# Kernel tuning notes

Measured on AMD Instinct MI355X. Metric: run time of the kernel, lower is better.

Reference implementation:

```python
import jax, jax.numpy as jnp
import numpy as np

N_NODES = 100000
N_EDGES = 1600000
IN_F = 512
OUT_F = 256
ORDER = 2


def setup_inputs() -> dict:
    key = jax.random.key(0)
    k1, k2, k3, k4, k5 = jax.random.split(key, 5)
    features = jax.random.normal(k1, (N_NODES, IN_F), dtype=jnp.float32)
    # Xavier-uniform init like torch.nn.init.xavier_uniform_
    limit = float(np.sqrt(6.0 / (IN_F + OUT_F)))
    weight = jax.random.uniform(k2, (IN_F, OUT_F), dtype=jnp.float32, minval=-limit, maxval=limit)
    row = jnp.sort(jax.random.randint(k3, (N_EDGES,), 0, N_NODES, dtype=jnp.int32))
    col = jax.random.randint(k4, (N_EDGES,), 0, N_NODES, dtype=jnp.int32)
    adj_vals = jax.random.uniform(k5, (N_EDGES,), dtype=jnp.float32)
    return {"features": features, "weight": weight, "row": row, "col": col, "adj_vals": adj_vals}


def _spmm(row, col, vals, x, n):
    # out[i] = sum_{e: row[e]==i} vals[e] * x[col[e]]  (COO sparse @ dense)
    msgs = vals[:, None] * x[col]  # [E, F]
    return jax.ops.segment_sum(msgs, row, num_segments=n)


def reference(features, weight, row, col, adj_vals):
    out = jnp.tanh(features @ weight)  # dense mm + tanh (active=True)
    for _ in range(ORDER):  # spmm once, then order-1 more times
        out = _spmm(row, col, adj_vals, out, N_NODES)
    return out
```

## Files before the change

### kernel.cpp

```cpp
#include <hip/hip_runtime.h>
#include <hip/hip_bf16.h>

#define M_NODES 100000
#define N_EDGES 1600000
#define K_IN 512
#define N_OUT 256

typedef short bf16x8 __attribute__((ext_vector_type(8)));
typedef float f32x4 __attribute__((ext_vector_type(4)));

#define GLOBAL_AS __attribute__((address_space(1)))
#define LDS_AS __attribute__((address_space(3)))

__device__ inline unsigned short f2bf_u(float f) {
  union { float f; unsigned u; } x; x.f = f;
  unsigned r = x.u + 0x7FFFu + ((x.u >> 16) & 1u);
  return (unsigned short)(r >> 16);
}
__device__ inline float bfu2f(unsigned short h) {
  union { unsigned u; float f; } x; x.u = ((unsigned)h) << 16;
  return x.f;
}

__global__ void prep_w_kernel(const float* __restrict__ w, short* __restrict__ wt) {
  int idx = blockIdx.x * 256 + threadIdx.x;
  int k = idx >> 8, n = idx & 255;
  wt[n * K_IN + k] = (short)f2bf_u(w[idx]);
}

__global__ void build_rp_kernel(const int* __restrict__ row, int* __restrict__ rp) {
  int r = blockIdx.x * 256 + threadIdx.x;
  if (r > M_NODES) return;
  int lo = 0, hi = N_EDGES;
  while (lo < hi) {
    int mid = (lo + hi) >> 1;
    if (row[mid] < r) lo = mid + 1; else hi = mid;
  }
  rp[r] = lo;
}

__global__ __launch_bounds__(256) void gemm_tanh_kernel(
    const float* __restrict__ A, const short* __restrict__ Wt,
    unsigned short* __restrict__ H) {
  __shared__ __align__(16) short As[64 * 64];
  __shared__ __align__(16) short Bs[256 * 64];
  const int tid = threadIdx.x;
  const int wave = tid >> 6, lane = tid & 63;
  const int quad = lane >> 4, l16 = lane & 15;
  const int row0 = blockIdx.x * 64;

  f32x4 acc[16];
  #pragma unroll
  for (int i = 0; i < 16; ++i) acc[i] = (f32x4){0.f, 0.f, 0.f, 0.f};

  const int ra = tid >> 2;
  const int kb = (tid & 3) << 4;
  const int gr = min(row0 + ra, M_NODES - 1);
  const float* Arow = A + (size_t)gr * K_IN;

  for (int k0 = 0; k0 < K_IN; k0 += 64) {
    #pragma unroll
    for (int it = 0; it < 8; ++it) {
      int g = wave * 512 + it * 64 + lane;
      int n = g >> 3, phys = g & 7;
      int j = phys ^ (n & 7);
      const short* gp = Wt + (size_t)n * K_IN + k0 + j * 8;
      __builtin_amdgcn_global_load_lds(
          (GLOBAL_AS const void*)gp,
          (LDS_AS void*)&Bs[(wave * 512 + it * 64) * 8],
          16, 0, 0);
    }
    float4 a0 = *(const float4*)&Arow[k0 + kb];
    float4 a1 = *(const float4*)&Arow[k0 + kb + 4];
    float4 a2 = *(const float4*)&Arow[k0 + kb + 8];
    float4 a3 = *(const float4*)&Arow[k0 + kb + 12];
    union { unsigned short s[16]; int4 v[2]; } u;
    u.s[0]=f2bf_u(a0.x); u.s[1]=f2bf_u(a0.y); u.s[2]=f2bf_u(a0.z); u.s[3]=f2bf_u(a0.w);
    u.s[4]=f2bf_u(a1.x); u.s[5]=f2bf_u(a1.y); u.s[6]=f2bf_u(a1.z); u.s[7]=f2bf_u(a1.w);
    u.s[8]=f2bf_u(a2.x); u.s[9]=f2bf_u(a2.y); u.s[10]=f2bf_u(a2.z); u.s[11]=f2bf_u(a2.w);
    u.s[12]=f2bf_u(a3.x); u.s[13]=f2bf_u(a3.y); u.s[14]=f2bf_u(a3.z); u.s[15]=f2bf_u(a3.w);
    int lc0 = kb >> 3;
    #pragma unroll
    for (int c = 0; c < 2; ++c) {
      int phys = (lc0 + c) ^ (ra & 7);
      *(int4*)&As[ra * 64 + phys * 8] = u.v[c];
    }
    __syncthreads();
    const int r = wave * 16 + l16;
    #pragma unroll
    for (int kstep = 0; kstep < 2; ++kstep) {
      int lc = kstep * 4 + quad;
      bf16x8 af = *(const bf16x8*)&As[r * 64 + (lc ^ (r & 7)) * 8];
      #pragma unroll
      for (int nt = 0; nt < 16; ++nt) {
        int n = nt * 16 + l16;
        bf16x8 bfr = *(const bf16x8*)&Bs[n * 64 + (lc ^ (n & 7)) * 8];
        acc[nt] = __builtin_amdgcn_mfma_f32_16x16x32_bf16(af, bfr, acc[nt], 0, 0, 0);
      }
    }
    __syncthreads();
  }
  #pragma unroll
  for (int nt = 0; nt < 16; ++nt) {
    #pragma unroll
    for (int rr = 0; rr < 4; ++rr) {
      int row = row0 + wave * 16 + quad * 4 + rr;
      if (row < M_NODES) {
        H[(size_t)row * N_OUT + nt * 16 + l16] = f2bf_u(tanhf(acc[nt][rr]));
      }
    }
  }
}

__global__ __launch_bounds__(256) void spmm_bf_bf(
    const int* __restrict__ rp, const int* __restrict__ colv,
    const float* __restrict__ vals, const unsigned short* __restrict__ x,
    unsigned short* __restrict__ y) {
  int w = (blockIdx.x * 256 + threadIdx.x) >> 6;
  int lane = threadIdx.x & 63;
  int i = __builtin_amdgcn_readfirstlane(w);
  int s = rp[i], e = rp[i + 1];
  float a0 = 0.f, a1 = 0.f, a2 = 0.f, a3 = 0.f;
  const unsigned short* xl = x + lane * 4;
  for (int base = s; base < e; base += 64) {
    int nn = min(e - base, 64);
    int tl = min(base + lane, e - 1);
    int c_l = colv[tl];
    float v_l = vals[tl];
    int tt = 0;
    for (; tt + 8 <= nn; tt += 8) {
      ushort4 xv[8]; float vv[8];
      #pragma unroll
      for (int j = 0; j < 8; ++j) {
        int c = __shfl(c_l, tt + j);
        vv[j] = __shfl(v_l, tt + j);
        xv[j] = *(const ushort4*)(xl + (size_t)c * N_OUT);
      }
      #pragma unroll
      for (int j = 0; j < 8; ++j) {
        a0 += vv[j] * bfu2f(xv[j].x); a1 += vv[j] * bfu2f(xv[j].y);
        a2 += vv[j] * bfu2f(xv[j].z); a3 += vv[j] * bfu2f(xv[j].w);
      }
    }
    for (; tt + 4 <= nn; tt += 4) {
      ushort4 xv[4]; float vv[4];
      #pragma unroll
      for (int j = 0; j < 4; ++j) {
        int c = __shfl(c_l, tt + j);
        vv[j] = __shfl(v_l, tt + j);
        xv[j] = *(const ushort4*)(xl + (size_t)c * N_OUT);
      }
      #pragma unroll
      for (int j = 0; j < 4; ++j) {
        a0 += vv[j] * bfu2f(xv[j].x); a1 += vv[j] * bfu2f(xv[j].y);
        a2 += vv[j] * bfu2f(xv[j].z); a3 += vv[j] * bfu2f(xv[j].w);
      }
    }
    for (; tt < nn; ++tt) {
      int c = __shfl(c_l, tt);
      float v = __shfl(v_l, tt);
      ushort4 xv = *(const ushort4*)(xl + (size_t)c * N_OUT);
      a0 += v * bfu2f(xv.x); a1 += v * bfu2f(xv.y);
      a2 += v * bfu2f(xv.z); a3 += v * bfu2f(xv.w);
    }
  }
  ushort4 o;
  o.x = f2bf_u(a0); o.y = f2bf_u(a1); o.z = f2bf_u(a2); o.w = f2bf_u(a3);
  *(ushort4*)(y + (size_t)i * N_OUT + lane * 4) = o;
}

__global__ __launch_bounds__(256) void spmm_bf_f32(
    const int* __restrict__ rp, const int* __restrict__ colv,
    const float* __restrict__ vals, const unsigned short* __restrict__ x,
    float* __restrict__ y) {
  int w = (blockIdx.x * 256 + threadIdx.x) >> 6;
  int lane = threadIdx.x & 63;
  int i = __builtin_amdgcn_readfirstlane(w);
  int s = rp[i], e = rp[i + 1];
  float a0 = 0.f, a1 = 0.f, a2 = 0.f, a3 = 0.f;
  const unsigned short* xl = x + lane * 4;
  for (int base = s; base < e; base += 64) {
    int nn = min(e - base, 64);
    int tl = min(base + lane, e - 1);
    int c_l = colv[tl];
    float v_l = vals[tl];
    int tt = 0;
    for (; tt + 8 <= nn; tt += 8) {
      ushort4 xv[8]; float vv[8];
      #pragma unroll
      for (int j = 0; j < 8; ++j) {
        int c = __shfl(c_l, tt + j);
        vv[j] = __shfl(v_l, tt + j);
        xv[j] = *(const ushort4*)(xl + (size_t)c * N_OUT);
      }
      #pragma unroll
      for (int j = 0; j < 8; ++j) {
        a0 += vv[j] * bfu2f(xv[j].x); a1 += vv[j] * bfu2f(xv[j].y);
        a2 += vv[j] * bfu2f(xv[j].z); a3 += vv[j] * bfu2f(xv[j].w);
      }
    }
    for (; tt + 4 <= nn; tt += 4) {
      ushort4 xv[4]; float vv[4];
      #pragma unroll
      for (int j = 0; j < 4; ++j) {
        int c = __shfl(c_l, tt + j);
        vv[j] = __shfl(v_l, tt + j);
        xv[j] = *(const ushort4*)(xl + (size_t)c * N_OUT);
      }
      #pragma unroll
      for (int j = 0; j < 4; ++j) {
        a0 += vv[j] * bfu2f(xv[j].x); a1 += vv[j] * bfu2f(xv[j].y);
        a2 += vv[j] * bfu2f(xv[j].z); a3 += vv[j] * bfu2f(xv[j].w);
      }
    }
    for (; tt < nn; ++tt) {
      int c = __shfl(c_l, tt);
      float v = __shfl(v_l, tt);
      ushort4 xv = *(const ushort4*)(xl + (size_t)c * N_OUT);
      a0 += v * bfu2f(xv.x); a1 += v * bfu2f(xv.y);
      a2 += v * bfu2f(xv.z); a3 += v * bfu2f(xv.w);
    }
  }
  float4 o = {a0, a1, a2, a3};
  *(float4*)(y + (size_t)i * N_OUT + lane * 4) = o;
}

extern "C" void kernel_launch(void* const* d_in, const int* in_sizes, int n_in,
                              void* d_out, int out_size, void* d_ws, size_t ws_size,
                              hipStream_t stream) {
  const float* features = (const float*)d_in[0];
  const float* weight   = (const float*)d_in[1];
  const int*   row      = (const int*)d_in[2];
  const int*   col      = (const int*)d_in[3];
  const float* vals     = (const float*)d_in[4];
  float* out = (float*)d_out;

  char* ws = (char*)d_ws;
  const size_t HB = (size_t)M_NODES * N_OUT * 2;
  const size_t RPB = 400016;
  unsigned short* H  = (unsigned short*)ws;
  unsigned short* y1 = (unsigned short*)(ws + HB);
  int*   rp = (int*)(ws + 2 * HB);
  short* Wt = (short*)(ws + 2 * HB + RPB);

  prep_w_kernel<<<512, 256, 0, stream>>>(weight, Wt);
  build_rp_kernel<<<(M_NODES + 1 + 255) / 256, 256, 0, stream>>>(row, rp);
  gemm_tanh_kernel<<<(M_NODES + 63) / 64, 256, 0, stream>>>(features, Wt, H);
  spmm_bf_bf<<<25000, 256, 0, stream>>>(rp, col, vals, H, y1);
  spmm_bf_f32<<<25000, 256, 0, stream>>>(rp, col, vals, y1, out);
}
```

Measured before the change: 603.2 us.

## Restructure GEMM to load weights directly from global with double-buffered A tile

Result: no change. 598.9 us (-0.7%).

```diff
diff --git a/kernel.cpp b/kernel.cpp
--- a/kernel.cpp
+++ b/kernel.cpp
@@ -20,6 +20,12 @@
 __device__ inline float bfu2f(unsigned short h) {
   union { unsigned u; float f; } x; x.u = ((unsigned)h) << 16;
   return x.f;
+}
+__device__ inline float fast_tanh(float x) {
+  float ax = __builtin_fabsf(x);
+  float z = __expf(-2.0f * ax);
+  float t = (1.0f - z) * __builtin_amdgcn_rcpf(1.0f + z);
+  return __builtin_copysignf(t, x);
 }
 
 __global__ void prep_w_kernel(const float* __restrict__ w, short* __restrict__ wt) {
@@ -39,74 +45,100 @@
   rp[r] = lo;
 }
 
-__global__ __launch_bounds__(256) void gemm_tanh_kernel(
+__global__ __launch_bounds__(256, 4) void gemm_tanh_kernel(
     const float* __restrict__ A, const short* __restrict__ Wt,
     unsigned short* __restrict__ H) {
-  __shared__ __align__(16) short As[64 * 64];
-  __shared__ __align__(16) short Bs[256 * 64];
+  __shared__ __align__(16) short As[2][64 * 64];
   const int tid = threadIdx.x;
   const int wave = tid >> 6, lane = tid & 63;
   const int quad = lane >> 4, l16 = lane & 15;
   const int row0 = blockIdx.x * 64;
 
-  f32x4 acc[16];
+  f32x4 acc[4][4];
   #pragma unroll
-  for (int i = 0; i < 16; ++i) acc[i] = (f32x4){0.f, 0.f, 0.f, 0.f};
+  for (int m = 0; m < 4; ++m)
+    #pragma unroll
+    for (int n = 0; n < 4; ++n) acc[m][n] = (f32x4){0.f, 0.f, 0.f, 0.f};
 
   const int ra = tid >> 2;
   const int kb = (tid & 3) << 4;
+  const int lc0 = kb >> 3;
   const int gr = min(row0 + ra, M_NODES - 1);
   const float* Arow = A + (size_t)gr * K_IN;
-
-  for (int k0 = 0; k0 < K_IN; k0 += 64) {
-    #pragma unroll
-    for (int it = 0; it < 8; ++it) {
-      int g = wave * 512 + it * 64 + lane;
-      int n = g >> 3, phys = g & 7;
-      int j = phys ^ (n & 7);
-      const short* gp = Wt + (size_t)n * K_IN + k0 + j * 8;
-      __builtin_amdgcn_global_load_lds(
-          (GLOBAL_AS const void*)gp,
-          (LDS_AS void*)&Bs[(wave * 512 + it * 64) * 8],
-          16, 0, 0);
-    }
-    float4 a0 = *(const float4*)&Arow[k0 + kb];
-    float4 a1 = *(const float4*)&Arow[k0 + kb + 4];
-    float4 a2 = *(const float4*)&Arow[k0 + kb + 8];
-    float4 a3 = *(const float4*)&Arow[k0 + kb + 12];
+  const short* Wb = Wt + (size_t)(wave * 64 + l16) * K_IN + quad * 8;
+
+  {
+    float4 a0 = *(const float4*)&Arow[kb];
+    float4 a1 = *(const float4*)&Arow[kb + 4];
+    float4 a2 = *(const float4*)&Arow[kb + 8];
+    float4 a3 = *(const float4*)&Arow[kb + 12];
     union { unsigned short s[16]; int4 v[2]; } u;
     u.s[0]=f2bf_u(a0.x); u.s[1]=f2bf_u(a0.y); u.s[2]=f2bf_u(a0.z); u.s[3]=f2bf_u(a0.w);
     u.s[4]=f2bf_u(a1.x); u.s[5]=f2bf_u(a1.y); u.s[6]=f2bf_u(a1.z); u.s[7]=f2bf_u(a1.w);
     u.s[8]=f2bf_u(a2.x); u.s[9]=f2bf_u(a2.y); u.s[10]=f2bf_u(a2.z); u.s[11]=f2bf_u(a2.w);
     u.s[12]=f2bf_u(a3.x); u.s[13]=f2bf_u(a3.y); u.s[14]=f2bf_u(a3.z); u.s[15]=f2bf_u(a3.w);
-    int lc0 = kb >> 3;
     #pragma unroll
     for (int c = 0; c < 2; ++c) {
       int phys = (lc0 + c) ^ (ra & 7);
-      *(int4*)&As[ra * 64 + phys * 8] = u.v[c];
+      *(int4*)&As[0][ra * 64 + phys * 8] = u.v[c];
+    }
+  }
+  __syncthreads();
+
+  int cur = 0;
+  for (int k0 = 0; k0 < K_IN; k0 += 64) {
+    float4 p0, p1, p2, p3;
+    const bool more = (k0 + 64) < K_IN;
+    if (more) {
+      p0 = *(const float4*)&Arow[k0 + 64 + kb];
+      p1 = *(const float4*)&Arow[k0 + 64 + kb + 4];
+      p2 = *(const float4*)&Arow[k0 + 64 + kb + 8];
+      p3 = *(const float4*)&Arow[k0 + 64 + kb + 12];
+    }
+    #pragma unroll
+    for (int kh = 0; kh < 2; ++kh) {
+      bf16x8 af[4];
+      #pragma unroll
+      for (int m = 0; m < 4; ++m) {
+        int r = m * 16 + l16;
+        int phys = (kh * 4 + quad) ^ (l16 & 7);
+        af[m] = *(const bf16x8*)&As[cur][r * 64 + phys * 8];
+      }
+      #pragma unroll
+      for (int nt = 0; nt < 4; ++nt) {
+        bf16x8 bfr = *(const bf16x8*)(Wb + (size_t)nt * 16 * K_IN + k0 + kh * 32);
+        #pragma unroll
+        for (int m = 0; m < 4; ++m)
+          acc[m][nt] = __builtin_amdgcn_mfma_f32_16x16x32_bf16(af[m], bfr, acc[m][nt], 0, 0, 0);
+      }
+    }
+    if (more) {
+      union { unsigned short s[16]; int4 v[2]; } u;
+      u.s[0]=f2bf_u(p0.x); u.s[1]=f2bf_u(p0.y); u.s[2]=f2bf_u(p0.z); u.s[3]=f2bf_u(p0.w);
+      u.s[4]=f2bf_u(p1.x); u.s[5]=f2bf_u(p1.y); u.s[6]=f2bf_u(p1.z); u.s[7]=f2bf_u(p1.w);
+      u.s[8]=f2bf_u(p2.x); u.s[9]=f2bf_u(p2.y); u.s[10]=f2bf_u(p2.z); u.s[11]=f2bf_u(p2.w);
+      u.s[12]=f2bf_u(p3.x); u.s[13]=f2bf_u(p3.y); u.s[14]=f2bf_u(p3.z); u.s[15]=f2bf_u(p3.w);
+      #pragma unroll
+      for (int c = 0; c < 2; ++c) {
+        int phys = (lc0 + c) ^ (ra & 7);
+        *(int4*)&As[cur ^ 1][ra * 64 + phys * 8] = u.v[c];
+      }
     }
     __syncthreads();
-    const int r = wave * 16 + l16;
-    #pragma unroll
-    for (int kstep = 0; kstep < 2; ++kstep) {
-      int lc = kstep * 4 + quad;
-      bf16x8 af = *(const bf16x8*)&As[r * 64 + (lc ^ (r & 7)) * 8];
-      #pragma unroll
-      for (int nt = 0; nt < 16; ++nt) {
-        int n = nt * 16 + l16;
-        bf16x8 bfr = *(const bf16x8*)&Bs[n * 64 + (lc ^ (n & 7)) * 8];
-        acc[nt] = __builtin_amdgcn_mfma_f32_16x16x32_bf16(af, bfr, acc[nt], 0, 0, 0);
-      }
-    }
-    __syncthreads();
-  }
+    cur ^= 1;
+  }
+
   #pragma unroll
-  for (int nt = 0; nt < 16; ++nt) {
+  for (int m = 0; m < 4; ++m) {
     #pragma unroll
     for (int rr = 0; rr < 4; ++rr) {
-      int row = row0 + wave * 16 + quad * 4 + rr;
+      int row = row0 + m * 16 + quad * 4 + rr;
       if (row < M_NODES) {
-        H[(size_t)row * N_OUT + nt * 16 + l16] = f2bf_u(tanhf(acc[nt][rr]));
+        #pragma unroll
+        for (int nt = 0; nt < 4; ++nt) {
+          H[(size_t)row * N_OUT + wave * 64 + nt * 16 + l16] =
+              f2bf_u(fast_tanh(acc[m][nt][rr]));
+        }
       }
     }
   }
```

## Drop LDS staging in GEMM; waves read A and B fragments directly from global

Applied to the files above, without the earlier changes.

Measured after the change: 649.5 us. 7.7% more time.

```diff
diff --git a/kernel.cpp b/kernel.cpp
--- a/kernel.cpp
+++ b/kernel.cpp
@@ -9,9 +9,6 @@
 typedef short bf16x8 __attribute__((ext_vector_type(8)));
 typedef float f32x4 __attribute__((ext_vector_type(4)));
 
-#define GLOBAL_AS __attribute__((address_space(1)))
-#define LDS_AS __attribute__((address_space(3)))
-
 __device__ inline unsigned short f2bf_u(float f) {
   union { float f; unsigned u; } x; x.f = f;
   unsigned r = x.u + 0x7FFFu + ((x.u >> 16) & 1u);
@@ -20,6 +17,12 @@
 __device__ inline float bfu2f(unsigned short h) {
   union { unsigned u; float f; } x; x.u = ((unsigned)h) << 16;
   return x.f;
+}
+__device__ inline float fast_tanh(float x) {
+  float ax = __builtin_fabsf(x);
+  float z = __expf(-2.0f * ax);
+  float t = (1.0f - z) * __builtin_amdgcn_rcpf(1.0f + z);
+  return __builtin_copysignf(t, x);
 }
 
 __global__ void prep_w_kernel(const float* __restrict__ w, short* __restrict__ wt) {
@@ -39,74 +42,74 @@
   rp[r] = lo;
 }
 
-__global__ __launch_bounds__(256) void gemm_tanh_kernel(
+__global__ __launch_bounds__(256, 2) void gemm_tanh_kernel(
     const float* __restrict__ A, const short* __restrict__ Wt,
     unsigned short* __restrict__ H) {
-  __shared__ __align__(16) short As[64 * 64];
-  __shared__ __align__(16) short Bs[256 * 64];
   const int tid = threadIdx.x;
   const int wave = tid >> 6, lane = tid & 63;
   const int quad = lane >> 4, l16 = lane & 15;
-  const int row0 = blockIdx.x * 64;
-
-  f32x4 acc[16];
+  const int R0 = (blockIdx.x * 4 + wave) * 32;
+
+  f32x4 acc[2][16];
   #pragma unroll
-  for (int i = 0; i < 16; ++i) acc[i] = (f32x4){0.f, 0.f, 0.f, 0.f};
-
-  const int ra = tid >> 2;
-  const int kb = (tid & 3) << 4;
-  const int gr = min(row0 + ra, M_NODES - 1);
-  const float* Arow = A + (size_t)gr * K_IN;
-
-  for (int k0 = 0; k0 < K_IN; k0 += 64) {
+  for (int m = 0; m < 2; ++m)
     #pragma unroll
-    for (int it = 0; it < 8; ++it) {
-      int g = wave * 512 + it * 64 + lane;
-      int n = g >> 3, phys = g & 7;
-      int j = phys ^ (n & 7);
-      const short* gp = Wt + (size_t)n * K_IN + k0 + j * 8;
-      __builtin_amdgcn_global_load_lds(
-          (GLOBAL_AS const void*)gp,
-          (LDS_AS void*)&Bs[(wave * 512 + it * 64) * 8],
-          16, 0, 0);
-    }
-    float4 a0 = *(const float4*)&Arow[k0 + kb];
-    float4 a1 = *(const float4*)&Arow[k0 + kb + 4];
-    float4 a2 = *(const float4*)&Arow[k0 + kb + 8];
-    float4 a3 = *(const float4*)&Arow[k0 + kb + 12];
-    union { unsigned short s[16]; int4 v[2]; } u;
-    u.s[0]=f2bf_u(a0.x); u.s[1]=f2bf_u(a0.y); u.s[2]=f2bf_u(a0.z); u.s[3]=f2bf_u(a0.w);
-    u.s[4]=f2bf_u(a1.x); u.s[5]=f2bf_u(a1.y); u.s[6]=f2bf_u(a1.z); u.s[7]=f2bf_u(a1.w);
-    u.s[8]=f2bf_u(a2.x); u.s[9]=f2bf_u(a2.y); u.s[10]=f2bf_u(a2.z); u.s[11]=f2bf_u(a2.w);
-    u.s[12]=f2bf_u(a3.x); u.s[13]=f2bf_u(a3.y); u.s[14]=f2bf_u(a3.z); u.s[15]=f2bf_u(a3.w);
-    int lc0 = kb >> 3;
+    for (int n = 0; n < 16; ++n) acc[m][n] = (f32x4){0.f, 0.f, 0.f, 0.f};
+
+  const float* Ab0;
+  const float* Ab1;
+  {
+    int g0 = min(R0 + l16, M_NODES - 1);
+    int g1 = min(R0 + 16 + l16, M_NODES - 1);
+    Ab0 = A + (size_t)g0 * K_IN + quad * 8;
+    Ab1 = A + (size_t)g1 * K_IN + quad * 8;
+  }
+  const short* Bb = Wt + (size_t)l16 * K_IN + quad * 8;
+
+  float4 a00 = *(const float4*)(Ab0);
+  float4 a01 = *(const float4*)(Ab0 + 4);
+  float4 a10 = *(const float4*)(Ab1);
+  float4 a11 = *(const float4*)(Ab1 + 4);
+
+  for (int ks = 0; ks < 16; ++ks) {
+    bf16x8 af0, af1;
+    {
+      union { unsigned short s[8]; bf16x8 v; } u;
+      u.s[0]=f2bf_u(a00.x); u.s[1]=f2bf_u(a00.y); u.s[2]=f2bf_u(a00.z); u.s[3]=f2bf_u(a00.w);
+      u.s[4]=f2bf_u(a01.x); u.s[5]=f2bf_u(a01.y); u.s[6]=f2bf_u(a01.z); u.s[7]=f2bf_u(a01.w);
+      af0 = u.v;
+      u.s[0]=f2bf_u(a10.x); u.s[1]=f2bf_u(a10.y); u.s[2]=f2bf_u(a10.z); u.s[3]=f2bf_u(a10.w);
+      u.s[4]=f2bf_u(a11.x); u.s[5]=f2bf_u(a11.y); u.s[6]=f2bf_u(a11.z); u.s[7]=f2bf_u(a11.w);
+      af1 = u.v;
+    }
+    if (ks < 15) {
+      const float* p0 = Ab0 + (ks + 1) * 32;
+      const float* p1 = Ab1 + (ks + 1) * 32;
+      a00 = *(const float4*)(p0);
+      a01 = *(const float4*)(p0 + 4);
+      a10 = *(const float4*)(p1);
+      a11 = *(const float4*)(p1 + 4);
+    }
+    const short* Bk = Bb + ks * 32;
     #pragma unroll
-    for (int c = 0; c < 2; ++c) {
-      int phys = (lc0 + c) ^ (ra & 7);
-      *(int4*)&As[ra * 64 + phys * 8] = u.v[c];
-    }
-    __syncthreads();
-    const int r = wave * 16 + l16;
-    #pragma unroll
-    for (int kstep = 0; kstep < 2; ++kstep) {
-      int lc = kstep * 4 + quad;
-      bf16x8 af = *(const bf16x8*)&As[r * 64 + (lc ^ (r & 7)) * 8];
-      #pragma unroll
-      for (int nt = 0; nt < 16; ++nt) {
-        int n = nt * 16 + l16;
-        bf16x8 bfr = *(const bf16x8*)&Bs[n * 64 + (lc ^ (n & 7)) * 8];
-        acc[nt] = __builtin_amdgcn_mfma_f32_16x16x32_bf16(af, bfr, acc[nt], 0, 0, 0);
-      }
-    }
-    __syncthreads();
-  }
+    for (int nt = 0; nt < 16; ++nt) {
+      bf16x8 bfr = *(const bf16x8*)(Bk + (size_t)nt * 16 * K_IN);
+      acc[0][nt] = __builtin_amdgcn_mfma_f32_16x16x32_bf16(af0, bfr, acc[0][nt], 0, 0, 0);
+      acc[1][nt] = __builtin_amdgcn_mfma_f32_16x16x32_bf16(af1, bfr, acc[1][nt], 0, 0, 0);
+    }
+  }
+
   #pragma unroll
-  for (int nt = 0; nt < 16; ++nt) {
+  for (int m = 0; m < 2; ++m) {
     #pragma unroll
     for (int rr = 0; rr < 4; ++rr) {
-      int row = row0 + wave * 16 + quad * 4 + rr;
+      int row = R0 + m * 16 + quad * 4 + rr;
       if (row < M_NODES) {
-        H[(size_t)row * N_OUT + nt * 16 + l16] = f2bf_u(tanhf(acc[nt][rr]));
+        #pragma unroll
+        for (int nt = 0; nt < 16; ++nt) {
+          H[(size_t)row * N_OUT + nt * 16 + l16] =
+              f2bf_u(fast_tanh(acc[m][nt][rr]));
+        }
       }
     }
   }
@@ -245,7 +248,7 @@
 
   prep_w_kernel<<<512, 256, 0, stream>>>(weight, Wt);
   build_rp_kernel<<<(M_NODES + 1 + 255) / 256, 256, 0, stream>>>(row, rp);
-  gemm_tanh_kernel<<<(M_NODES + 63) / 64, 256, 0, stream>>>(features, Wt, H);
+  gemm_tanh_kernel<<<(M_NODES + 127) / 128, 256, 0, stream>>>(features, Wt, H);
   spmm_bf_bf<<<25000, 256, 0, stream>>>(rp, col, vals, H, y1);
   spmm_bf_f32<<<25000, 256, 0, stream>>>(rp, col, vals, y1, out);
 }
```
